# Kernel tuning notes

Measured on AMD Instinct MI355X. Metric: run time of the kernel, lower is better.

Reference implementation:

```python
import jax, jax.numpy as jnp
import numpy as np

D_STATE = 16
D_CONV = 4
DT_RANK = 8


def layer_norm(x, g, b, eps=1e-5):
    m = x.mean(-1, keepdims=True)
    v = ((x - m) ** 2).mean(-1, keepdims=True)
    return (x - m) / jnp.sqrt(v + eps) * g + b


def rms_norm(x, w, eps=1e-5):
    return x * jax.lax.rsqrt(jnp.mean(x * x, -1, keepdims=True) + eps) * w


def mamba_layer(feat, in_proj_w, conv_w, conv_b, x_proj_w, dt_proj_w, dt_proj_b,
                A_log, D_param, out_proj_w, rms_w):
    # feat: [N, C] treated as a length-N sequence with batch 1 (residual block)
    x_in = rms_norm(feat, rms_w)
    xz = x_in @ in_proj_w                         # [N, 2*d_inner]
    d_inner = conv_w.shape[0]
    x, z = xz[:, :d_inner], xz[:, d_inner:]
    # causal depthwise conv1d (torch pad=d_conv-1 then truncate to L)
    L = x.shape[0]
    x_pad = jnp.pad(x, ((D_CONV - 1, 0), (0, 0)))
    xc = conv_b + sum(x_pad[k:k + L, :] * conv_w[:, k] for k in range(D_CONV))
    x = jax.nn.silu(xc)
    dbc = x @ x_proj_w                            # [N, dt_rank + 2*d_state]
    delta = jax.nn.softplus(dbc[:, :DT_RANK] @ dt_proj_w + dt_proj_b)  # [N, d_inner]
    Bm = dbc[:, DT_RANK:DT_RANK + D_STATE]        # [N, d_state]
    Cm = dbc[:, DT_RANK + D_STATE:]               # [N, d_state]
    A = -jnp.exp(A_log)                           # [d_inner, d_state]

    def step(h, inp):
        d_t, b_t, c_t, x_t = inp
        dA = jnp.exp(d_t[:, None] * A)            # [d_inner, d_state]
        h = dA * h + d_t[:, None] * b_t[None, :] * x_t[:, None]
        y_t = (h * c_t[None, :]).sum(-1)          # [d_inner]
        return h, y_t

    h0 = jnp.zeros((d_inner, D_STATE), feat.dtype)
    _, y = jax.lax.scan(step, h0, (delta, Bm, Cm, x))
    y = y + D_param * x
    y = y * jax.nn.silu(z)
    return feat + y @ out_proj_w                  # residual


def setup_inputs() -> dict:
    N, K, C = 32768, 16, 128
    d_inner = 2 * C
    key = jax.random.key(0)
    ks = jax.random.split(key, 12)
    s = 0.02
    inp = {
        "feat": jax.random.normal(ks[0], (N, C), jnp.float32),
        "coord": jax.random.normal(ks[1], (N, 3), jnp.float32),
        "reference_index": jax.random.randint(ks[2], (N, K), 0, N, jnp.int32),
        "gauss_dist": jax.random.uniform(ks[3], (N, K), jnp.float32),
        "j": 0,
        # Mamba params
        "in_proj_w": jax.random.normal(ks[4], (C, 2 * d_inner), jnp.float32) * s,
        "conv_w": jax.random.normal(ks[5], (d_inner, D_CONV), jnp.float32) * s,
        "conv_b": jnp.zeros((d_inner,), jnp.float32),
        "x_proj_w": jax.random.normal(ks[6], (d_inner, DT_RANK + 2 * D_STATE), jnp.float32) * s,
        "dt_proj_w": jax.random.normal(ks[7], (DT_RANK, d_inner), jnp.float32) * s,
        "dt_proj_b": jax.random.uniform(ks[8], (d_inner,), jnp.float32) * 0.1,
        "A_log": jnp.log(jnp.tile(jnp.arange(1.0, D_STATE + 1.0, dtype=jnp.float32), (d_inner, 1))),
        "D_param": jnp.ones((d_inner,), jnp.float32),
        "out_proj_w": jax.random.normal(ks[9], (d_inner, C), jnp.float32) * s,
        "rms_w": jnp.ones((C,), jnp.float32),
        # PointBatchNorm (LayerNorm) shared for both norms
        "ln_g": jnp.ones((C,), jnp.float32),
        "ln_b": jnp.zeros((C,), jnp.float32),
        # linear_attention: Linear(2C->C), LayerNorm, ReLU, Linear(C->C)
        "la_w1": jax.random.normal(ks[10], (2 * C, C), jnp.float32) * s,
        "la_b1": jnp.zeros((C,), jnp.float32),
        "la_ln_g": jnp.ones((C,), jnp.float32),
        "la_ln_b": jnp.zeros((C,), jnp.float32),
        "la_w2": jax.random.normal(ks[11], (C, C), jnp.float32) * s,
        "la_b2": jnp.zeros((C,), jnp.float32),
    }
    return inp


def reference(feat, coord, reference_index, gauss_dist, j,
              in_proj_w, conv_w, conv_b, x_proj_w, dt_proj_w, dt_proj_b,
              A_log, D_param, out_proj_w, rms_w, ln_g, ln_b,
              la_w1, la_b1, la_ln_g, la_ln_b, la_w2, la_b2):
    # pointops.grouping(with_xyz=False): gather neighbor features [N, K, C]
    group_feat = feat[reference_index]
    combined = (gauss_dist[..., None] * group_feat).sum(axis=1)     # [N, C]
    combined = layer_norm(combined, ln_g, ln_b)
    feat_mamba = mamba_layer(feat, in_proj_w, conv_w, conv_b, x_proj_w,
                             dt_proj_w, dt_proj_b, A_log, D_param,
                             out_proj_w, rms_w)
    feat_mamba = layer_norm(feat_mamba, ln_g, ln_b)
    cat_feat = jnp.concatenate([feat_mamba, combined], axis=-1)     # [N, 2C]
    h = jax.nn.relu(layer_norm(cat_feat @ la_w1 + la_b1, la_ln_g, la_ln_b))
    return h @ la_w2 + la_b2
```

## Files before the change

### kernel.cpp

```cpp
#include <hip/hip_runtime.h>
#include <hip/hip_bf16.h>
#include <math.h>

#define N_TOK 32768
#define LC 32
#define NCHUNK (N_TOK / LC)
#define NSEG 64
#define SEGLEN (NCHUNK / NSEG)
#define CXT 16
#define NCXB (N_TOK / CXT)
#define NGRP 8192
#define G_CXD 2048
#define G_S1  4096
#define G_S2  2048
#define XPAD 264

typedef short short8 __attribute__((ext_vector_type(8)));
typedef float f32x4 __attribute__((ext_vector_type(4)));

__device__ __forceinline__ float siluf_(float v){ return v / (1.f + __expf(-v)); }
__device__ __forceinline__ float softplusf_(float v){ return v > 20.f ? v : __logf(1.f + __expf(v)); }

__device__ __forceinline__ unsigned f2bfu(float f){
  __hip_bfloat16 h = __float2bfloat16(f);
  return (unsigned)*(unsigned short*)&h;
}
__device__ __forceinline__ float bfu2f(unsigned short u){
  __hip_bfloat16 h; *(unsigned short*)&h = u; return __bfloat162float(h);
}

__device__ __forceinline__ float waveRed64(float v){
  #pragma unroll
  for (int m = 1; m < 64; m <<= 1) v += __shfl_xor(v, m);
  return v;
}

__device__ __forceinline__ void pow_chain(float w, float pw[16]){
  pw[0]=w; pw[1]=w*w; pw[2]=pw[1]*w; pw[3]=pw[1]*pw[1];
  pw[4]=pw[3]*pw[0]; pw[5]=pw[3]*pw[1]; pw[6]=pw[3]*pw[2]; pw[7]=pw[3]*pw[3];
  pw[8]=pw[7]*pw[0]; pw[9]=pw[7]*pw[1]; pw[10]=pw[7]*pw[2]; pw[11]=pw[7]*pw[3];
  pw[12]=pw[7]*pw[4]; pw[13]=pw[7]*pw[5]; pw[14]=pw[7]*pw[6]; pw[15]=pw[7]*pw[7];
}

__device__ __forceinline__ bool check_intA(const float aS[16]){
  bool ok = true;
  #pragma unroll
  for (int s=0;s<16;s++){
    float tgt = (float)(s+1);
    if (fabsf(-aS[s] - tgt) > 1e-4f*tgt) ok = false;
  }
  return ok;
}

__device__ __forceinline__ void gather_ln(int grp, int tid,
      const unsigned* __restrict__ fb16u, const int* __restrict__ ridx,
      const float* __restrict__ gd, const float* __restrict__ g,
      const float* __restrict__ b, unsigned* __restrict__ catB){
  int row = grp*4 + (tid>>6);
  int lane = tid & 63;
  float ax=0.f, ay=0.f;
  #pragma unroll 4
  for (int k=0;k<16;k++){
    int idx = ridx[row*16+k];
    float ww = gd[row*16+k];
    unsigned fu = fb16u[(size_t)idx*64 + lane];
    ax += ww*bfu2f((unsigned short)(fu & 0xffff));
    ay += ww*bfu2f((unsigned short)(fu >> 16));
  }
  float m = waveRed64(ax+ay) * (1.f/128.f);
  float dx = ax-m, dy = ay-m;
  float var = waveRed64(dx*dx+dy*dy) * (1.f/128.f);
  float is = rsqrtf(var + 1e-5f);
  float2 gg = ((const float2*)g)[lane];
  float2 bb = ((const float2*)b)[lane];
  float ox = dx*is*gg.x + bb.x, oy = dy*is*gg.y + bb.y;
  catB[row*64 + lane] = f2bfu(ox) | (f2bfu(oy) << 16);
}

__global__ void __launch_bounds__(256) k_front(const float* __restrict__ feat,
                        const float* __restrict__ rmsw,
                        unsigned* __restrict__ a0u, unsigned* __restrict__ fb16u,
                        const float* __restrict__ ipw, const float* __restrict__ opw,
                        const float* __restrict__ w1, const float* __restrict__ w2,
                        const float* __restrict__ xpw,
                        __hip_bfloat16* __restrict__ ipwt, __hip_bfloat16* __restrict__ opwt,
                        __hip_bfloat16* __restrict__ w1t, __hip_bfloat16* __restrict__ w2t,
                        __hip_bfloat16* __restrict__ xpwt){
  int bid = blockIdx.x;
  if (bid >= 8192){
    int e = (bid-8192)*256 + threadIdx.x;
    if (e < 65536){ int n=e>>7, k=e&127; ipwt[e]=__float2bfloat16(ipw[k*512+n]); }
    else if (e < 98304){ int f=e-65536; int n=f>>8, k=f&255; opwt[f]=__float2bfloat16(opw[k*128+n]); }
    else if (e < 131072){ int f=e-98304; int n=f>>8, k=f&255; w1t[f]=__float2bfloat16(w1[k*128+n]); }
    else if (e < 147456){ int f=e-131072; int n=f>>7, k=f&127; w2t[f]=__float2bfloat16(w2[k*128+n]); }
    else if (e < 159744){ int f=e-147456; int n=f>>8, k=f&255;
                          xpwt[f]=(n<40)?__float2bfloat16(xpw[k*40+n]):__float2bfloat16(0.f); }
    return;
  }
  int row = bid*4 + (threadIdx.x>>6);
  int lane = threadIdx.x & 63;
  float2 f2 = ((const float2*)feat)[row*64 + lane];
  fb16u[row*64 + lane] = f2bfu(f2.x) | (f2bfu(f2.y) << 16);
  float ss = waveRed64(f2.x*f2.x + f2.y*f2.y);
  float is0 = rsqrtf(ss * (1.f/128.f) + 1e-5f);
  float2 w = ((const float2*)rmsw)[lane];
  a0u[row*64 + lane] = f2bfu(f2.x*is0*w.x) | (f2bfu(f2.y*is0*w.y) << 16);
}

template<int WM16, int WN16>
__global__ __launch_bounds__(256) void k_mfma(const __hip_bfloat16* __restrict__ A,
      const __hip_bfloat16* __restrict__ Wt, int K,
      __hip_bfloat16* __restrict__ out0b, __hip_bfloat16* __restrict__ out1){
  int tid = threadIdx.x;
  int wave = tid>>6, lane = tid&63;
  int wm = wave>>1, wn = wave&1;
  int lane16 = lane&15, quad = lane>>4;
  int m_w = blockIdx.x*(2*WM16*16) + wm*(WM16*16);
  int n_w = blockIdx.y*(2*WN16*16) + wn*(WN16*16);
  f32x4 acc[WM16][WN16];
  #pragma unroll
  for (int i=0;i<WM16;i++)
    #pragma unroll
    for (int j=0;j<WN16;j++) acc[i][j] = (f32x4){0.f,0.f,0.f,0.f};
  const __hip_bfloat16* Ab = A  + (size_t)(m_w + lane16)*K + quad*8;
  const __hip_bfloat16* Bb = Wt + (size_t)(n_w + lane16)*K + quad*8;
  #pragma unroll 4
  for (int kk=0; kk<K; kk+=32){
    short8 a[WM16], b[WN16];
    #pragma unroll
    for (int i=0;i<WM16;i++) a[i] = *(const short8*)(Ab + (size_t)i*16*K + kk);
    #pragma unroll
    for (int j=0;j<WN16;j++) b[j] = *(const short8*)(Bb + (size_t)j*16*K + kk);
    #pragma unroll
    for (int i=0;i<WM16;i++)
      #pragma unroll
      for (int j=0;j<WN16;j++)
        acc[i][j] = __builtin_amdgcn_mfma_f32_16x16x32_bf16(b[j], a[i], acc[i][j], 0, 0, 0);
  }
  #pragma unroll
  for (int i=0;i<WM16;i++){
    int m = m_w + i*16 + lane16;
    #pragma unroll
    for (int j=0;j<WN16;j++){
      int n0 = n_w + j*16 + quad*4;
      if (n0 < 256){
        unsigned u0 = f2bfu(acc[i][j][0]) | (f2bfu(acc[i][j][1]) << 16);
        unsigned u1 = f2bfu(acc[i][j][2]) | (f2bfu(acc[i][j][3]) << 16);
        *(uint2*)(out0b + (size_t)m*256 + n0) = make_uint2(u0, u1);
      } else {
        unsigned u0 = f2bfu(siluf_(acc[i][j][0])) | (f2bfu(siluf_(acc[i][j][1])) << 16);
        unsigned u1 = f2bfu(siluf_(acc[i][j][2])) | (f2bfu(siluf_(acc[i][j][3])) << 16);
        *(uint2*)(out1 + (size_t)m*256 + (n0-256)) = make_uint2(u0, u1);
      }
    }
  }
}

__global__ __launch_bounds__(256) void k_cxd(
      const __hip_bfloat16* __restrict__ bxb,
      const __hip_bfloat16* __restrict__ xpwt,
      const float* __restrict__ cw, const float* __restrict__ cb,
      const float* __restrict__ dtw, const float* __restrict__ dtb,
      unsigned* __restrict__ dxb,
      float* __restrict__ Bm, float* __restrict__ Cm,
      const unsigned* __restrict__ fb16u, const int* __restrict__ ridx,
      const float* __restrict__ gd, const float* __restrict__ g,
      const float* __restrict__ b, unsigned* __restrict__ catB){
  int tid = threadIdx.x;
  int bid = blockIdx.x;

  if (bid >= NCXB){
    gather_ln(bid - NCXB, tid, fb16u, ridx, gd, g, b, catB);
    return;
  }

  __shared__ __align__(16) __hip_bfloat16 Xs[CXT][XPAD];
  __shared__ __align__(16) float DT[CXT][8];
  int wave = tid>>6, lane = tid&63;
  int lane16 = lane&15, quad = lane>>4;
  int r0 = bid*CXT;

  {
    int d = tid;
    float cw0=cw[d*4], cw1=cw[d*4+1], cw2=cw[d*4+2], cw3=cw[d*4+3], cbb=cb[d];
    float a_0 = (r0 >= 3) ? __bfloat162float(bxb[(size_t)(r0-3)*256 + d]) : 0.f;
    float a_1 = (r0 >= 2) ? __bfloat162float(bxb[(size_t)(r0-2)*256 + d]) : 0.f;
    float a_2 = (r0 >= 1) ? __bfloat162float(bxb[(size_t)(r0-1)*256 + d]) : 0.f;
    #pragma unroll 4
    for (int t=0;t<CXT;t++){
      float a_3 = __bfloat162float(bxb[(size_t)(r0+t)*256 + d]);
      float xc = siluf_(cbb + cw0*a_0 + cw1*a_1 + cw2*a_2 + cw3*a_3);
      Xs[t][d] = __float2bfloat16(xc);
      a_0=a_1; a_1=a_2; a_2=a_3;
    }
  }
  __syncthreads();

  if (wave < 3){
    f32x4 acc3 = (f32x4){0.f,0.f,0.f,0.f};
    const __hip_bfloat16* Arow = &Xs[lane16][0] + quad*8;
    const __hip_bfloat16* Bb = xpwt + (size_t)(wave*16 + lane16)*256 + quad*8;
    #pragma unroll
    for (int kk=0; kk<256; kk+=32){
      short8 a  = *(const short8*)(Arow + kk);
      short8 bfr = *(const short8*)(Bb + kk);
      acc3 = __builtin_amdgcn_mfma_f32_16x16x32_bf16(a, bfr, acc3, 0, 0, 0);
    }
    int n = wave*16 + lane16;
    #pragma unroll
    for (int r=0;r<4;r++){
      int m = quad*4 + r;
      float v = acc3[r];
      if (n < 8)       DT[m][n] = v;
      else if (n < 24) Bm[(size_t)(r0+m)*16 + (n-8)] = v;
      else if (n < 40) Cm[(size_t)(r0+m)*16 + (n-24)] = v;
    }
  }
  __syncthreads();

  {
    int d = tid;
    float w8[8];
    #pragma unroll
    for (int j=0;j<8;j++) w8[j] = dtw[j*256+d];
    float dbias = dtb[d];
    #pragma unroll
    for (int t=0;t<CXT;t++){
      const float4* T = (const float4*)&DT[t][0];
      float4 u = T[0], v = T[1];
      float acc = dbias
        + u.x*w8[0] + u.y*w8[1] + u.z*w8[2] + u.w*w8[3]
        + v.x*w8[4] + v.y*w8[5] + v.z*w8[6] + v.w*w8[7];
      float dv = softplusf_(acc);
      unsigned xu = *(const unsigned short*)&Xs[t][d];
      dxb[(size_t)(r0+t)*256 + d] = f2bfu(dv) | (xu << 16);
    }
  }
}

__global__ __launch_bounds__(256) void k_scan1(const unsigned* __restrict__ dxb,
      const float* __restrict__ Bm, const float* __restrict__ A_log,
      float* __restrict__ dsum_o, __hip_bfloat16* __restrict__ Hc,
      const unsigned* __restrict__ fb16u, const int* __restrict__ ridx,
      const float* __restrict__ gd, const float* __restrict__ g,
      const float* __restrict__ b, unsigned* __restrict__ catB){
  __shared__ float Bl[LC][16];
  int g_ = blockIdx.x;
  int tid = threadIdx.x;
  if (g_ >= NCHUNK){
    gather_ln(G_CXD + (g_ - NCHUNK), tid, fb16u, ridx, gd, g, b, catB);
    return;
  }
  int d = tid;
  int t0 = g_*LC;
  if (tid < LC*4) ((float4*)&Bl[0][0])[tid] = ((const float4*)(Bm + (size_t)t0*16))[tid];
  __syncthreads();
  float aS[16];
  #pragma unroll
  for (int s=0;s<16;s++) aS[s] = -__expf(A_log[d*16+s]);
  bool fastA = check_intA(aS);
  float h[16] = {};
  float dsum = 0.f;
  if (fastA){
    #pragma unroll 4
    for (int t=0;t<LC;t++){
      unsigned u = dxb[(size_t)(t0+t)*256 + d];
      float dv = bfu2f((unsigned short)(u & 0xffff));
      float xv = bfu2f((unsigned short)(u >> 16));
      const float4* Bp = (const float4*)&Bl[t][0];
      float4 b0=Bp[0], b1=Bp[1], b2=Bp[2], b3=Bp[3];
      float bl[16] = {b0.x,b0.y,b0.z,b0.w, b1.x,b1.y,b1.z,b1.w,
                      b2.x,b2.y,b2.z,b2.w, b3.x,b3.y,b3.z,b3.w};
      dsum += dv;
      float dx_ = dv*xv;
      float w[16]; pow_chain(__expf(-dv), w);
      #pragma unroll
      for (int s=0;s<16;s++) h[s] = w[s]*h[s] + dx_*bl[s];
    }
  } else {
    #pragma unroll 4
    for (int t=0;t<LC;t++){
      unsigned u = dxb[(size_t)(t0+t)*256 + d];
      float dv = bfu2f((unsigned short)(u & 0xffff));
      float xv = bfu2f((unsigned short)(u >> 16));
      const float4* Bp = (const float4*)&Bl[t][0];
      float4 b0=Bp[0], b1=Bp[1], b2=Bp[2], b3=Bp[3];
      float bl[16] = {b0.x,b0.y,b0.z,b0.w, b1.x,b1.y,b1.z,b1.w,
                      b2.x,b2.y,b2.z,b2.w, b3.x,b3.y,b3.z,b3.w};
      dsum += dv;
      float dx_ = dv*xv;
      #pragma unroll
      for (int s=0;s<16;s++) h[s] = __expf(dv*aS[s])*h[s] + dx_*bl[s];
    }
  }
  dsum_o[(size_t)g_*256 + d] = dsum;
  unsigned u[8];
  #pragma unroll
  for (int q=0;q<8;q++) u[q] = f2bfu(h[2*q]) | (f2bfu(h[2*q+1]) << 16);
  uint4* Hd = (uint4*)(Hc + (size_t)g_*4096 + (size_t)d*16);
  Hd[0] = make_uint4(u[0],u[1],u[2],u[3]);
  Hd[1] = make_uint4(u[4],u[5],u[6],u[7]);
}

__global__ __launch_bounds__(256) void k_carry_a(const float* __restrict__ dsum,
      __hip_bfloat16* __restrict__ Hc, const float* __restrict__ A_log,
      float* __restrict__ dsum_pre, float* __restrict__ segsum, float* __restrict__ Hagg){
  int seg = blockIdx.x;
  int ch  = blockIdx.y*256 + threadIdx.x;
  int d = ch>>4, s = ch&15;
  float aSv = -__expf(A_log[ch]);
  float dpre = 0.f, c = 0.f;
  int g0 = seg*SEGLEN;
  #pragma unroll 4
  for (int i=0;i<SEGLEN;i++){
    int g = g0+i;
    float ds = dsum[(size_t)g*256 + d];
    size_t a = (size_t)g*4096 + ch;
    float hh = __bfloat162float(Hc[a]);
    float p = __expf(ds*aSv);
    if (s==0) dsum_pre[(size_t)g*256 + d] = dpre;
    Hc[a] = __float2bfloat16(c);
    dpre += ds;
    c = p*c + hh;
  }
  if (s==0) segsum[seg*256 + d] = dpre;
  Hagg[(size_t)seg*4096 + ch] = c;
}

__global__ __launch_bounds__(256) void k_carry_b(const float* __restrict__ segsum,
      const float* __restrict__ Hagg, const float* __restrict__ A_log,
      float* __restrict__ Cseg){
  int ch = blockIdx.x*256 + threadIdx.x;
  int d = ch>>4;
  float aSv = -__expf(A_log[ch]);
  float c = 0.f;
  #pragma unroll 8
  for (int s=0;s<NSEG;s++){
    Cseg[(size_t)s*4096 + ch] = c;
    c = __expf(segsum[s*256 + d]*aSv)*c + Hagg[(size_t)s*4096 + ch];
  }
}

__global__ __launch_bounds__(256) void k_scan2(const unsigned* __restrict__ dxb,
      const __hip_bfloat16* __restrict__ zb, const float* __restrict__ Bm,
      const float* __restrict__ Cm, const float* __restrict__ A_log,
      const float* __restrict__ Dp, const float* __restrict__ dsum_pre,
      const __hip_bfloat16* __restrict__ Hc, const float* __restrict__ Cseg,
      __hip_bfloat16* __restrict__ yb,
      const unsigned* __restrict__ fb16u, const int* __restrict__ ridx,
      const float* __restrict__ gd, const float* __restrict__ g,
      const float* __restrict__ b, unsigned* __restrict__ catB){
  __shared__ float Bl[LC][16];
  __shared__ float Cl[LC][16];
  int g_ = blockIdx.x;
  int tid = threadIdx.x;
  if (g_ >= NCHUNK){
    gather_ln(G_CXD + G_S1 + (g_ - NCHUNK), tid, fb16u, ridx, gd, g, b, catB);
    return;
  }
  int d = tid;
  int t0 = g_*LC;
  if (tid < 128) ((float4*)&Bl[0][0])[tid] = ((const float4*)(Bm + (size_t)t0*16))[tid];
  else ((float4*)&Cl[0][0])[tid-128] = ((const float4*)(Cm + (size_t)t0*16))[tid-128];
  __syncthreads();
  int seg = g_ / SEGLEN;
  float aS[16];
  #pragma unroll
  for (int s=0;s<16;s++) aS[s] = -__expf(A_log[d*16+s]);
  bool fastA = check_intA(aS);
  float h[16];
  {
    float dpre = dsum_pre[(size_t)g_*256 + d];
    const uint4* hp = (const uint4*)(Hc + (size_t)g_*4096 + (size_t)d*16);
    uint4 H0 = hp[0], H1 = hp[1];
    unsigned hu[8] = {H0.x,H0.y,H0.z,H0.w, H1.x,H1.y,H1.z,H1.w};
    const float4* cs = (const float4*)(Cseg + (size_t)seg*4096 + (size_t)d*16);
    float ws[16];
    if (fastA){
      pow_chain(__expf(-dpre), ws);
    } else {
      #pragma unroll
      for (int s=0;s<16;s++) ws[s] = __expf(dpre*aS[s]);
    }
    #pragma unroll
    for (int q=0;q<4;q++){
      float4 C = cs[q];
      h[q*4+0] = ws[q*4+0]*C.x + bfu2f((unsigned short)(hu[q*2]   & 0xffff));
      h[q*4+1] = ws[q*4+1]*C.y + bfu2f((unsigned short)(hu[q*2]   >> 16));
      h[q*4+2] = ws[q*4+2]*C.z + bfu2f((unsigned short)(hu[q*2+1] & 0xffff));
      h[q*4+3] = ws[q*4+3]*C.w + bfu2f((unsigned short)(hu[q*2+1] >> 16));
    }
  }
  float dpar = Dp[d];
  if (fastA){
    #pragma unroll 4
    for (int t=0;t<LC;t++){
      unsigned u = dxb[(size_t)(t0+t)*256 + d];
      float dv = bfu2f((unsigned short)(u & 0xffff));
      float xv = bfu2f((unsigned short)(u >> 16));
      float zv = __bfloat162float(zb[(size_t)(t0+t)*256 + d]);
      const float4* Bp = (const float4*)&Bl[t][0];
      const float4* Cp = (const float4*)&Cl[t][0];
      float4 b0=Bp[0], b1=Bp[1], b2=Bp[2], b3=Bp[3];
      float4 c0=Cp[0], c1=Cp[1], c2=Cp[2], c3=Cp[3];
      float bl[16] = {b0.x,b0.y,b0.z,b0.w, b1.x,b1.y,b1.z,b1.w,
                      b2.x,b2.y,b2.z,b2.w, b3.x,b3.y,b3.z,b3.w};
      float cl[16] = {c0.x,c0.y,c0.z,c0.w, c1.x,c1.y,c1.z,c1.w,
                      c2.x,c2.y,c2.z,c2.w, c3.x,c3.y,c3.z,c3.w};
      float dx_ = dv*xv;
      float w[16]; pow_chain(__expf(-dv), w);
      float yv = 0.f;
      #pragma unroll
      for (int s=0;s<16;s++){
        h[s] = w[s]*h[s] + dx_*bl[s];
        yv += h[s]*cl[s];
      }
      yb[(size_t)(t0+t)*256 + d] = __float2bfloat16((yv + dpar*xv)*zv);
    }
  } else {
    #pragma unroll 4
    for (int t=0;t<LC;t++){
      unsigned u = dxb[(size_t)(t0+t)*256 + d];
      float dv = bfu2f((unsigned short)(u & 0xffff));
      float xv = bfu2f((unsigned short)(u >> 16));
      float zv = __bfloat162float(zb[(size_t)(t0+t)*256 + d]);
      const float4* Bp = (const float4*)&Bl[t][0];
      const float4* Cp = (const float4*)&Cl[t][0];
      float4 b0=Bp[0], b1=Bp[1], b2=Bp[2], b3=Bp[3];
      float4 c0=Cp[0], c1=Cp[1], c2=Cp[2], c3=Cp[3];
      float bl[16] = {b0.x,b0.y,b0.z,b0.w, b1.x,b1.y,b1.z,b1.w,
                      b2.x,b2.y,b2.z,b2.w, b3.x,b3.y,b3.z,b3.w};
      float cl[16] = {c0.x,c0.y,c0.z,c0.w, c1.x,c1.y,c1.z,c1.w,
                      c2.x,c2.y,c2.z,c2.w, c3.x,c3.y,c3.z,c3.w};
      float dx_ = dv*xv;
      float yv = 0.f;
      #pragma unroll
      for (int s=0;s<16;s++){
        h[s] = __expf(dv*aS[s])*h[s] + dx_*bl[s];
        yv += h[s]*cl[s];
      }
      yb[(size_t)(t0+t)*256 + d] = __float2bfloat16((yv + dpar*xv)*zv);
    }
  }
}

__global__ __launch_bounds__(256) void k_tail(const __hip_bfloat16* __restrict__ yb,
      const __hip_bfloat16* __restrict__ opwt, const float* __restrict__ feat,
      const float* __restrict__ lng, const float* __restrict__ lnb,
      const unsigned* __restrict__ catB,
      const __hip_bfloat16* __restrict__ w1t, const float* __restrict__ b1,
      const float* __restrict__ lag, const float* __restrict__ lab,
      const __hip_bfloat16* __restrict__ w2t, const float* __restrict__ b2,
      float* __restrict__ out){
  __shared__ __align__(16) float Ls[64][132];
  __shared__ __align__(16) unsigned Cu[64][132];
  int tid = threadIdx.x;
  int wave = tid>>6, lane = tid&63;
  int wm = wave>>1, wn = wave&1;
  int lane16 = lane&15, quad = lane>>4;
  int r0 = blockIdx.x*64;

  #pragma unroll
  for (int i=0;i<16;i++){
    int idx = i*256 + tid;
    int row = idx>>6, c = idx&63;
    Cu[row][64+c] = catB[(size_t)(r0+row)*64 + c];
  }

  f32x4 acc[2][4];
  #pragma unroll
  for (int i=0;i<2;i++)
    #pragma unroll
    for (int j=0;j<4;j++) acc[i][j] = (f32x4){0.f,0.f,0.f,0.f};
  {
    const __hip_bfloat16* Ab = yb   + (size_t)(r0 + wm*32 + lane16)*256 + quad*8;
    const __hip_bfloat16* Bb = opwt + (size_t)(wn*64 + lane16)*256 + quad*8;
    #pragma unroll 2
    for (int kk=0; kk<256; kk+=32){
      short8 a[2], bf[4];
      #pragma unroll
      for (int i=0;i<2;i++) a[i] = *(const short8*)(Ab + (size_t)i*16*256 + kk);
      #pragma unroll
      for (int j=0;j<4;j++) bf[j] = *(const short8*)(Bb + (size_t)j*16*256 + kk);
      #pragma unroll
      for (int i=0;i<2;i++)
        #pragma unroll
        for (int j=0;j<4;j++)
          acc[i][j] = __builtin_amdgcn_mfma_f32_16x16x32_bf16(a[i], bf[j], acc[i][j], 0, 0, 0);
    }
  }
  #pragma unroll
  for (int i=0;i<2;i++)
    #pragma unroll
    for (int j=0;j<4;j++){
      int n = wn*64 + j*16 + lane16;
      #pragma unroll
      for (int r=0;r<4;r++){
        int m = wm*32 + i*16 + quad*4 + r;
        Ls[m][n] = acc[i][j][r] + feat[(size_t)(r0+m)*128 + n];
      }
    }
  __syncthreads();
  {
    float2 gv = ((const float2*)lng)[lane];
    float2 bv = ((const float2*)lnb)[lane];
    #pragma unroll 4
    for (int rr=0; rr<16; rr++){
      int row = wave*16 + rr;
      float2 v = *(const float2*)&Ls[row][2*lane];
      float mm = waveRed64(v.x+v.y) * (1.f/128.f);
      float dx = v.x-mm, dy = v.y-mm;
      float var = waveRed64(dx*dx+dy*dy) * (1.f/128.f);
      float is = rsqrtf(var + 1e-5f);
      Cu[row][lane] = f2bfu(dx*is*gv.x + bv.x) | (f2bfu(dy*is*gv.y + bv.y) << 16);
    }
  }
  __syncthreads();
  #pragma unroll
  for (int i=0;i<2;i++)
    #pragma unroll
    for (int j=0;j<4;j++) acc[i][j] = (f32x4){0.f,0.f,0.f,0.f};
  {
    const __hip_bfloat16* Bb = w1t + (size_t)(wn*64 + lane16)*256 + quad*8;
    #pragma unroll 2
    for (int kk=0; kk<256; kk+=32){
      short8 a[2], bf[4];
      #pragma unroll
      for (int i=0;i<2;i++)
        a[i] = *(const short8*)(&Cu[wm*32 + i*16 + lane16][0] + (kk>>1) + quad*4);
      #pragma unroll
      for (int j=0;j<4;j++) bf[j] = *(const short8*)(Bb + (size_t)j*16*256 + kk);
      #pragma unroll
      for (int i=0;i<2;i++)
        #pragma unroll
        for (int j=0;j<4;j++)
          acc[i][j] = __builtin_amdgcn_mfma_f32_16x16x32_bf16(a[i], bf[j], acc[i][j], 0, 0, 0);
    }
  }
  #pragma unroll
  for (int i=0;i<2;i++)
    #pragma unroll
    for (int j=0;j<4;j++){
      int n = wn*64 + j*16 + lane16;
      float bv1 = b1[n];
      #pragma unroll
      for (int r=0;r<4;r++){
        int m = wm*32 + i*16 + quad*4 + r;
        Ls[m][n] = acc[i][j][r] + bv1;
      }
    }
  __syncthreads();
  {
    float2 gv = ((const float2*)lag)[lane];
    float2 bv = ((const float2*)lab)[lane];
    #pragma unroll 4
    for (int rr=0; rr<16; rr++){
      int row = wave*16 + rr;
      float2 v = *(const float2*)&Ls[row][2*lane];
      float mm = waveRed64(v.x+v.y) * (1.f/128.f);
      float dx = v.x-mm, dy = v.y-mm;
      float var = waveRed64(dx*dx+dy*dy) * (1.f/128.f);
      float is = rsqrtf(var + 1e-5f);
      float ox = fmaxf(dx*is*gv.x + bv.x, 0.f);
      float oy = fmaxf(dy*is*gv.y + bv.y, 0.f);
      Cu[row][lane] = f2bfu(ox) | (f2bfu(oy) << 16);
    }
  }
  __syncthreads();
  #pragma unroll
  for (int i=0;i<2;i++)
    #pragma unroll
    for (int j=0;j<4;j++) acc[i][j] = (f32x4){0.f,0.f,0.f,0.f};
  {
    const __hip_bfloat16* Bb = w2t + (size_t)(wn*64 + lane16)*128 + quad*8;
    #pragma unroll
    for (int kk=0; kk<128; kk+=32){
      short8 a[2], bf[4];
      #pragma unroll
      for (int i=0;i<2;i++)
        a[i] = *(const short8*)(&Cu[wm*32 + i*16 + lane16][0] + (kk>>1) + quad*4);
      #pragma unroll
      for (int j=0;j<4;j++) bf[j] = *(const short8*)(Bb + (size_t)j*16*128 + kk);
      #pragma unroll
      for (int i=0;i<2;i++)
        #pragma unroll
        for (int j=0;j<4;j++)
          acc[i][j] = __builtin_amdgcn_mfma_f32_16x16x32_bf16(bf[j], a[i], acc[i][j], 0, 0, 0);
    }
  }
  #pragma unroll
  for (int i=0;i<2;i++){
    int m = wm*32 + i*16 + lane16;
    #pragma unroll
    for (int j=0;j<4;j++){
      int n0 = wn*64 + j*16 + quad*4;
      float4 o;
      o.x = acc[i][j][0] + b2[n0+0];
      o.y = acc[i][j][1] + b2[n0+1];
      o.z = acc[i][j][2] + b2[n0+2];
      o.w = acc[i][j][3] + b2[n0+3];
      *(float4*)(out + (size_t)(r0+m)*128 + n0) = o;
    }
  }
}

extern "C" void kernel_launch(void* const* d_in, const int* in_sizes, int n_in,
                              void* d_out, int out_size, void* d_ws, size_t ws_size,
                              hipStream_t stream){
  const float* feat = (const float*)d_in[0];
  const int*   ridx = (const int*)d_in[2];
  const float* gd   = (const float*)d_in[3];
  const float* ipw  = (const float*)d_in[5];
  const float* cw   = (const float*)d_in[6];
  const float* cb   = (const float*)d_in[7];
  const float* xpw  = (const float*)d_in[8];
  const float* dtw  = (const float*)d_in[9];
  const float* dtb  = (const float*)d_in[10];
  const float* alog = (const float*)d_in[11];
  const float* dpar = (const float*)d_in[12];
  const float* opw  = (const float*)d_in[13];
  const float* rmsw = (const float*)d_in[14];
  const float* lng  = (const float*)d_in[15];
  const float* lnb  = (const float*)d_in[16];
  const float* w1   = (const float*)d_in[17];
  const float* b1   = (const float*)d_in[18];
  const float* lag  = (const float*)d_in[19];
  const float* lab  = (const float*)d_in[20];
  const float* w2   = (const float*)d_in[21];
  const float* b2   = (const float*)d_in[22];
  float* out = (float*)d_out;

  char* p = (char*)d_ws;
  __hip_bfloat16* bxb  = (__hip_bfloat16*)p; p += (size_t)N_TOK*256*2;
  __hip_bfloat16* zb   = (__hip_bfloat16*)p; p += (size_t)N_TOK*256*2;
  unsigned* dxb        = (unsigned*)p;       p += (size_t)N_TOK*256*4;
  unsigned* catB       = (unsigned*)p;       p += (size_t)N_TOK*64*4;
  unsigned* fb16u      = (unsigned*)p;       p += (size_t)N_TOK*64*4;
  __hip_bfloat16* yb   = (__hip_bfloat16*)p; p += (size_t)N_TOK*256*2;
  float* Bm   = (float*)p; p += (size_t)N_TOK*16*4;
  float* Cm   = (float*)p; p += (size_t)N_TOK*16*4;
  __hip_bfloat16* Hc = (__hip_bfloat16*)p; p += (size_t)NCHUNK*4096*2;
  float* dsum = (float*)p; p += (size_t)NCHUNK*256*4;
  float* dpre = (float*)p; p += (size_t)NCHUNK*256*4;
  float* segs = (float*)p; p += (size_t)NSEG*256*4;
  float* Hagg = (float*)p; p += (size_t)NSEG*4096*4;
  float* Cseg = (float*)p; p += (size_t)NSEG*4096*4;
  __hip_bfloat16* ipwt = (__hip_bfloat16*)p; p += 512*128*2;
  __hip_bfloat16* opwt = (__hip_bfloat16*)p; p += 128*256*2;
  __hip_bfloat16* w1t  = (__hip_bfloat16*)p; p += 128*256*2;
  __hip_bfloat16* w2t  = (__hip_bfloat16*)p; p += 128*128*2;
  __hip_bfloat16* xpwt = (__hip_bfloat16*)p; p += 48*256*2;
  __hip_bfloat16* a0 = yb;

  hipLaunchKernelGGL(k_front, dim3(8192+624), dim3(256), 0, stream,
                     feat, rmsw, (unsigned*)a0, fb16u,
                     ipw, opw, w1, w2, xpw, ipwt, opwt, w1t, w2t, xpwt);
  hipLaunchKernelGGL((k_mfma<4,4>), dim3(N_TOK/128, 4), dim3(256), 0, stream,
                     a0, ipwt, 128, bxb, zb);
  hipLaunchKernelGGL(k_cxd, dim3(NCXB + G_CXD), dim3(256), 0, stream,
                     bxb, xpwt, cw, cb, dtw, dtb, dxb, Bm, Cm,
                     fb16u, ridx, gd, lng, lnb, catB);
  hipLaunchKernelGGL(k_scan1, dim3(NCHUNK + G_S1), dim3(256), 0, stream,
                     dxb, Bm, alog, dsum, Hc,
                     fb16u, ridx, gd, lng, lnb, catB);
  hipLaunchKernelGGL(k_carry_a, dim3(NSEG, 16), dim3(256), 0, stream,
                     dsum, Hc, alog, dpre, segs, Hagg);
  hipLaunchKernelGGL(k_carry_b, dim3(16), dim3(256), 0, stream, segs, Hagg, alog, Cseg);
  hipLaunchKernelGGL(k_scan2, dim3(NCHUNK + G_S2), dim3(256), 0, stream,
                     dxb, zb, Bm, Cm, alog, dpar, dpre, Hc, Cseg, yb,
                     fb16u, ridx, gd, lng, lnb, catB);
  hipLaunchKernelGGL(k_tail, dim3(N_TOK/64), dim3(256), 0, stream,
                     yb, opwt, feat, lng, lnb, catB, w1t, b1, lag, lab, w2t, b2, out);
}
```

Before: 265.8 us.

## Fold segment carry propagation into scan2 and drop carry_b kernel

Removes the serial k_carry_b launch, which runs on only 16 blocks and walks 64 segments in sequence. Each k_scan2 block now rebuilds its own segment carry by looping over all preceding segments' segsum and Hagg values. This saves one kernel launch plus a low-parallelism serial pass and the Cseg buffer round trip. The cost is redundant work: up to 63 iterations of exp/pow_chain and 64-byte loads per thread in every chunk block.

```diff
diff --git a/kernel.cpp b/kernel.cpp
--- a/kernel.cpp
+++ b/kernel.cpp
@@ -327,25 +327,12 @@
   Hagg[(size_t)seg*4096 + ch] = c;
 }
 
-__global__ __launch_bounds__(256) void k_carry_b(const float* __restrict__ segsum,
-      const float* __restrict__ Hagg, const float* __restrict__ A_log,
-      float* __restrict__ Cseg){
-  int ch = blockIdx.x*256 + threadIdx.x;
-  int d = ch>>4;
-  float aSv = -__expf(A_log[ch]);
-  float c = 0.f;
-  #pragma unroll 8
-  for (int s=0;s<NSEG;s++){
-    Cseg[(size_t)s*4096 + ch] = c;
-    c = __expf(segsum[s*256 + d]*aSv)*c + Hagg[(size_t)s*4096 + ch];
-  }
-}
-
 __global__ __launch_bounds__(256) void k_scan2(const unsigned* __restrict__ dxb,
       const __hip_bfloat16* __restrict__ zb, const float* __restrict__ Bm,
       const float* __restrict__ Cm, const float* __restrict__ A_log,
       const float* __restrict__ Dp, const float* __restrict__ dsum_pre,
-      const __hip_bfloat16* __restrict__ Hc, const float* __restrict__ Cseg,
+      const __hip_bfloat16* __restrict__ Hc,
+      const float* __restrict__ segsum, const float* __restrict__ Hagg,
       __hip_bfloat16* __restrict__ yb,
       const unsigned* __restrict__ fb16u, const int* __restrict__ ridx,
       const float* __restrict__ gd, const float* __restrict__ g,
@@ -368,13 +355,33 @@
   #pragma unroll
   for (int s=0;s<16;s++) aS[s] = -__expf(A_log[d*16+s]);
   bool fastA = check_intA(aS);
+
+  float cseg[16];
+  #pragma unroll
+  for (int s=0;s<16;s++) cseg[s] = 0.f;
+  for (int s2=0; s2<seg; s2++){
+    float ssv = segsum[s2*256 + d];
+    float wseg[16];
+    if (fastA){
+      pow_chain(__expf(-ssv), wseg);
+    } else {
+      #pragma unroll
+      for (int s=0;s<16;s++) wseg[s] = __expf(ssv*aS[s]);
+    }
+    const float4* hg = (const float4*)(Hagg + (size_t)s2*4096 + (size_t)d*16);
+    float4 g0=hg[0], g1=hg[1], g2=hg[2], g3=hg[3];
+    float hv[16] = {g0.x,g0.y,g0.z,g0.w, g1.x,g1.y,g1.z,g1.w,
+                    g2.x,g2.y,g2.z,g2.w, g3.x,g3.y,g3.z,g3.w};
+    #pragma unroll
+    for (int s=0;s<16;s++) cseg[s] = wseg[s]*cseg[s] + hv[s];
+  }
+
   float h[16];
   {
     float dpre = dsum_pre[(size_t)g_*256 + d];
     const uint4* hp = (const uint4*)(Hc + (size_t)g_*4096 + (size_t)d*16);
     uint4 H0 = hp[0], H1 = hp[1];
     unsigned hu[8] = {H0.x,H0.y,H0.z,H0.w, H1.x,H1.y,H1.z,H1.w};
-    const float4* cs = (const float4*)(Cseg + (size_t)seg*4096 + (size_t)d*16);
     float ws[16];
     if (fastA){
       pow_chain(__expf(-dpre), ws);
@@ -384,11 +391,10 @@
     }
     #pragma unroll
     for (int q=0;q<4;q++){
-      float4 C = cs[q];
-      h[q*4+0] = ws[q*4+0]*C.x + bfu2f((unsigned short)(hu[q*2]   & 0xffff));
-      h[q*4+1] = ws[q*4+1]*C.y + bfu2f((unsigned short)(hu[q*2]   >> 16));
-      h[q*4+2] = ws[q*4+2]*C.z + bfu2f((unsigned short)(hu[q*2+1] & 0xffff));
-      h[q*4+3] = ws[q*4+3]*C.w + bfu2f((unsigned short)(hu[q*2+1] >> 16));
+      h[q*4+0] = ws[q*4+0]*cseg[q*4+0] + bfu2f((unsigned short)(hu[q*2]   & 0xffff));
+      h[q*4+1] = ws[q*4+1]*cseg[q*4+1] + bfu2f((unsigned short)(hu[q*2]   >> 16));
+      h[q*4+2] = ws[q*4+2]*cseg[q*4+2] + bfu2f((unsigned short)(hu[q*2+1] & 0xffff));
+      h[q*4+3] = ws[q*4+3]*cseg[q*4+3] + bfu2f((unsigned short)(hu[q*2+1] >> 16));
     }
   }
   float dpar = Dp[d];
@@ -644,7 +650,6 @@
   float* dpre = (float*)p; p += (size_t)NCHUNK*256*4;
   float* segs = (float*)p; p += (size_t)NSEG*256*4;
   float* Hagg = (float*)p; p += (size_t)NSEG*4096*4;
-  float* Cseg = (float*)p; p += (size_t)NSEG*4096*4;
   __hip_bfloat16* ipwt = (__hip_bfloat16*)p; p += 512*128*2;
   __hip_bfloat16* opwt = (__hip_bfloat16*)p; p += 128*256*2;
   __hip_bfloat16* w1t  = (__hip_bfloat16*)p; p += 128*256*2;
@@ -665,9 +670,8 @@
                      fb16u, ridx, gd, lng, lnb, catB);
   hipLaunchKernelGGL(k_carry_a, dim3(NSEG, 16), dim3(256), 0, stream,
                      dsum, Hc, alog, dpre, segs, Hagg);
-  hipLaunchKernelGGL(k_carry_b, dim3(16), dim3(256), 0, stream, segs, Hagg, alog, Cseg);
   hipLaunchKernelGGL(k_scan2, dim3(NCHUNK + G_S2), dim3(256), 0, stream,
-                     dxb, zb, Bm, Cm, alog, dpar, dpre, Hc, Cseg, yb,
+                     dxb, zb, Bm, Cm, alog, dpar, dpre, Hc, segs, Hagg, yb,
                      fb16u, ridx, gd, lng, lnb, catB);
   hipLaunchKernelGGL(k_tail, dim3(N_TOK/64), dim3(256), 0, stream,
                      yb, opwt, feat, lng, lnb, catB, w1t, b1, lag, lab, w2t, b2, out);
```

After: 295.7 us. +11.2%, slower.
